# Optimization experiments

Hardware: AMD Instinct MI355X
Metric: run time of the kernel (lower is better)

## Reference

```python
import jax, jax.numpy as jnp
import numpy as np

B, F, N = 64, 32, 36
REGION, HIDDEN, ATT = 1024, 1024, 1024
FEAT2 = REGION + 2 * HIDDEN  # temp_attn feat_size = 3072


def setup_inputs() -> dict:
    key = jax.random.key(0)
    ks = jax.random.split(key, 12)
    s = 0.02
    return {
        "frame_feats": jax.random.normal(ks[0], (B, F, 2 * HIDDEN), jnp.float32),
        "object_feats": jax.random.normal(ks[1], (B, F, N, REGION), jnp.float32),
        "hidden_state": jax.random.normal(ks[2], (B, HIDDEN), jnp.float32),
        # spatial attention params (torch Linear: y = x @ W.T + b)
        "s_wh_w": jax.random.normal(ks[3], (ATT, HIDDEN), jnp.float32) * s,
        "s_wh_b": jnp.zeros((ATT,), jnp.float32),
        "s_wv_w": jax.random.normal(ks[4], (ATT, REGION), jnp.float32) * s,
        "s_wv_b": jnp.zeros((ATT,), jnp.float32),
        "s_wa_w": jax.random.normal(ks[5], (ATT,), jnp.float32) * s,
        # temporal attention params (att_size = hidden_size here)
        "t_wh_w": jax.random.normal(ks[6], (HIDDEN, HIDDEN), jnp.float32) * s,
        "t_wh_b": jnp.zeros((HIDDEN,), jnp.float32),
        "t_wv_w": jax.random.normal(ks[7], (HIDDEN, FEAT2), jnp.float32) * s,
        "t_wv_b": jnp.zeros((HIDDEN,), jnp.float32),
        "t_wa_w": jax.random.normal(ks[8], (HIDDEN,), jnp.float32) * s,
    }


def reference(frame_feats, object_feats, hidden_state,
              s_wh_w, s_wh_b, s_wv_w, s_wv_b, s_wa_w,
              t_wh_w, t_wh_b, t_wv_w, t_wv_b, t_wa_w):
    # ---- spatial attention over num_boxes, per (batch, frame) ----
    # v: [B,F,N,ATT]; key proj broadcasts over frames and boxes
    v = jnp.einsum('bfnd,ad->bfna', object_feats, s_wv_w) + s_wv_b
    h = hidden_state @ s_wh_w.T + s_wh_b            # [B,ATT]
    score = jnp.tanh(v + h[:, None, None, :]) @ s_wa_w  # [B,F,N]
    alpha = jax.nn.softmax(score, axis=-1)
    obj_att = jnp.einsum('bfn,bfnd->bfd', alpha, object_feats)  # [B,F,REGION]

    # ---- temporal attention over frames ----
    feat = jnp.concatenate([obj_att, frame_feats], axis=-1)     # [B,F,FEAT2]
    v2 = jnp.einsum('bfd,ad->bfa', feat, t_wv_w) + t_wv_b       # [B,F,HIDDEN]
    h2 = hidden_state @ t_wh_w.T + t_wh_b                       # [B,HIDDEN]
    score2 = jnp.tanh(v2 + h2[:, None, :]) @ t_wa_w             # [B,F]
    beta = jax.nn.softmax(score2, axis=-1)
    loc_feat = jnp.einsum('bf,bfd->bd', beta, feat)             # [B,FEAT2]
    return loc_feat
```

## Files before the change

kernel.cpp:

```cpp
#include <hip/hip_runtime.h>
#include <hip/hip_bf16.h>
#include <stdint.h>

#define BATCH  64
#define NFRAME 32
#define NBOX   36
#define REGION 1024
#define HIDDEN 1024
#define ATTSZ  1024
#define FEAT2  3072
#define M_S (BATCH * NFRAME * NBOX)
#define M_T (BATCH * NFRAME)

typedef __attribute__((ext_vector_type(8))) short bf16x8;
typedef __attribute__((ext_vector_type(4))) float f32x4;

__device__ __forceinline__ unsigned short f2bf(float f) {
  union { float f; uint32_t u; } v; v.f = f;
  return (unsigned short)((v.u + 0x7FFFu + ((v.u >> 16) & 1u)) >> 16);
}
__device__ __forceinline__ float bf2f(unsigned short u) {
  union { uint32_t u; float f; } v; v.u = (uint32_t)u << 16; return v.f;
}
__device__ __forceinline__ float fast_tanh(float x) {
  float e = __expf(2.f * x);
  return 1.f - 2.f / (e + 1.f);
}
__device__ __forceinline__ void gload_lds16(const unsigned short* g, unsigned short* l) {
  __builtin_amdgcn_global_load_lds(
      (const __attribute__((address_space(1))) unsigned int*)g,
      (__attribute__((address_space(3))) unsigned int*)l, 16, 0, 0);
}

__global__ __launch_bounds__(256) void cast_f32_bf16(
    const float* __restrict__ in, unsigned short* __restrict__ out, long n) {
  long i = ((long)blockIdx.x * 256 + threadIdx.x) * 8;
  if (i >= n) return;
  float4 a = *(const float4*)(in + i);
  float4 b = *(const float4*)(in + i + 4);
  ushort4 lo; lo.x = f2bf(a.x); lo.y = f2bf(a.y); lo.z = f2bf(a.z); lo.w = f2bf(a.w);
  ushort4 hi; hi.x = f2bf(b.x); hi.y = f2bf(b.y); hi.z = f2bf(b.z); hi.w = f2bf(b.w);
  *(ushort4*)(out + i) = lo;
  *(ushort4*)(out + i + 4) = hi;
}

#define BM 128
#define BN 128
#define BK 64

__global__ __launch_bounds__(256) void gemm_tanh_score_bf16(
    const unsigned short* __restrict__ A, const unsigned short* __restrict__ W,
    const float* __restrict__ hvec, const float* __restrict__ wa,
    float* __restrict__ score, int K, int rows_per_b, int n_col_tiles)
{
  __shared__ unsigned short ldsA[BM * BK];
  __shared__ unsigned short ldsW[BN * BK];
  __shared__ float h_tile[4][BN];
  __shared__ float score_sh[2][BM];

  const int tid  = threadIdx.x;
  const int lane = tid & 63;
  const int wid  = tid >> 6;
  const int wr   = (wid >> 1) * 64;
  const int wc   = (wid & 1) * 64;
  const int l15  = lane & 15;
  const int q    = lane >> 4;
  const long r0  = (long)blockIdx.y * BM;
  const int srow = lane >> 3;
  const int sgr  = lane & 7;

  const int b0 = (int)(r0 / rows_per_b);
  const int t1 = (b0 + 1) * rows_per_b - (int)r0;
  const int t2 = t1 + rows_per_b;
  const int t3 = t2 + rows_per_b;

  float sreg[4][4] = {};

  for (int t = 0; t < n_col_tiles; ++t) {
    const int c0 = (blockIdx.x * n_col_tiles + t) * BN;
    __syncthreads();
    for (int idx = tid; idx < 4 * BN; idx += 256) {
      int bl = idx >> 7, c = idx & 127;
      int b = b0 + bl; if (b > BATCH - 1) b = BATCH - 1;
      h_tile[bl][c] = hvec[(long)b * ATTSZ + c0 + c];
    }
    float wac[4];
    #pragma unroll
    for (int j = 0; j < 4; ++j) wac[j] = wa[c0 + wc + j * 16 + l15];

    f32x4 acc[4][4] = {};
    for (int k0 = 0; k0 < K; k0 += BK) {
      __syncthreads();
      #pragma unroll
      for (int it = 0; it < 4; ++it) {
        int c = wid * 4 + it;
        int row = c * 8 + srow;
        gload_lds16(A + (r0 + row) * (long)K + k0 + sgr * 8, ldsA + c * 512);
        gload_lds16(W + (long)(c0 + row) * K + k0 + sgr * 8, ldsW + c * 512);
      }
      __syncthreads();
      #pragma unroll
      for (int s = 0; s < 2; ++s) {
        bf16x8 af[4], wf[4];
        #pragma unroll
        for (int i = 0; i < 4; ++i)
          af[i] = *(const bf16x8*)(ldsA + (wr + i * 16 + l15) * 64 + s * 32 + q * 8);
        #pragma unroll
        for (int j = 0; j < 4; ++j)
          wf[j] = *(const bf16x8*)(ldsW + (wc + j * 16 + l15) * 64 + s * 32 + q * 8);
        #pragma unroll
        for (int i = 0; i < 4; ++i)
          #pragma unroll
          for (int j = 0; j < 4; ++j)
            acc[i][j] = __builtin_amdgcn_mfma_f32_16x16x32_bf16(af[i], wf[j], acc[i][j], 0, 0, 0);
      }
    }
    #pragma unroll
    for (int i = 0; i < 4; ++i) {
      #pragma unroll
      for (int r = 0; r < 4; ++r) {
        int lrow = wr + i * 16 + q * 4 + r;
        int bl = (lrow >= t1) + (lrow >= t2) + (lrow >= t3);
        float part = 0.f;
        #pragma unroll
        for (int j = 0; j < 4; ++j) {
          float x = acc[i][j][r] + h_tile[bl][wc + j * 16 + l15];
          part += fast_tanh(x) * wac[j];
        }
        sreg[i][r] += part;
      }
    }
  }
  #pragma unroll
  for (int i = 0; i < 4; ++i)
    #pragma unroll
    for (int r = 0; r < 4; ++r) {
      float v = sreg[i][r];
      v += __shfl_xor(v, 1); v += __shfl_xor(v, 2);
      v += __shfl_xor(v, 4); v += __shfl_xor(v, 8);
      sreg[i][r] = v;
    }
  if (l15 == 0) {
    #pragma unroll
    for (int i = 0; i < 4; ++i)
      #pragma unroll
      for (int r = 0; r < 4; ++r)
        score_sh[wid & 1][wr + i * 16 + q * 4 + r] = sreg[i][r];
  }
  __syncthreads();
  if (tid < BM)
    atomicAdd(score + r0 + tid, score_sh[0][tid] + score_sh[1][tid]);
}

__global__ __launch_bounds__(256) void hidden_proj(
    const float* __restrict__ hidden,
    const float* __restrict__ s_wh_w, const float* __restrict__ s_wh_b,
    const float* __restrict__ s_wv_b,
    const float* __restrict__ t_wh_w, const float* __restrict__ t_wh_b,
    const float* __restrict__ t_wv_b,
    float* __restrict__ h_s, float* __restrict__ h_t)
{
  const float *W, *b1, *b2;
  float* out;
  if (blockIdx.y == 0) { W = s_wh_w; b1 = s_wh_b; b2 = s_wv_b; out = h_s; }
  else                 { W = t_wh_w; b1 = t_wh_b; b2 = t_wv_b; out = h_t; }
  const int lane = threadIdx.x & 63;
  const int wid  = threadIdx.x >> 6;
  const int a    = blockIdx.x * 4 + wid;
  __shared__ float hs[64 * 256];
  float acc[64];
  #pragma unroll
  for (int b = 0; b < 64; ++b) acc[b] = 0.f;

  for (int dc = 0; dc < 4; ++dc) {
    __syncthreads();
    for (int i = threadIdx.x; i < 4096; i += 256) {
      int b = i >> 6, d4 = i & 63;
      *(float4*)(hs + b * 256 + d4 * 4) =
          *(const float4*)(hidden + b * 1024 + dc * 256 + d4 * 4);
    }
    __syncthreads();
    float4 w4 = *(const float4*)(W + (long)a * 1024 + dc * 256 + lane * 4);
    #pragma unroll
    for (int b = 0; b < 64; ++b) {
      float4 h4 = *(const float4*)(hs + b * 256 + lane * 4);
      acc[b] += w4.x * h4.x + w4.y * h4.y + w4.z * h4.z + w4.w * h4.w;
    }
  }
  #pragma unroll
  for (int b = 0; b < 64; ++b) {
    #pragma unroll
    for (int off = 1; off < 64; off <<= 1)
      acc[b] += __shfl_xor(acc[b], off);
  }
  float res = 0.f;
  #pragma unroll
  for (int b = 0; b < 64; ++b)
    if (lane == b) res = acc[b];
  out[lane * 1024 + a] = res + b1[a] + b2[a];
}

__global__ __launch_bounds__(256) void spatial_softmax_obj_bf16(
    const unsigned short* __restrict__ objb, const float* __restrict__ score,
    const float* __restrict__ frame, float* __restrict__ feat,
    unsigned short* __restrict__ featb)
{
  const int bf = blockIdx.x;
  __shared__ float alpha[NBOX];
  if (threadIdx.x < 64) {
    int n = threadIdx.x;
    float v = (n < NBOX) ? score[bf * NBOX + n] : -1e30f;
    float m = v;
    #pragma unroll
    for (int off = 32; off; off >>= 1) m = fmaxf(m, __shfl_xor(m, off));
    float e = (n < NBOX) ? __expf(v - m) : 0.f;
    float ssum = e;
    #pragma unroll
    for (int off = 32; off; off >>= 1) ssum += __shfl_xor(ssum, off);
    if (n < NBOX) alpha[n] = e / ssum;
  }
  __syncthreads();
  const unsigned short* base = objb + (long)bf * NBOX * REGION;
  float4 av = {0.f, 0.f, 0.f, 0.f};
  for (int n = 0; n < NBOX; ++n) {
    float al = alpha[n];
    ushort4 o = *(const ushort4*)(base + n * REGION + threadIdx.x * 4);
    av.x += al * bf2f(o.x); av.y += al * bf2f(o.y);
    av.z += al * bf2f(o.z); av.w += al * bf2f(o.w);
  }
  float* frow = feat + (long)bf * FEAT2;
  unsigned short* fbrow = featb + (long)bf * FEAT2;
  *(float4*)(frow + threadIdx.x * 4) = av;
  ushort4 avb; avb.x = f2bf(av.x); avb.y = f2bf(av.y); avb.z = f2bf(av.z); avb.w = f2bf(av.w);
  *(ushort4*)(fbrow + threadIdx.x * 4) = avb;
  const float* fsrc = frame + (long)bf * 2 * HIDDEN;
  #pragma unroll
  for (int c = 0; c < 2; ++c) {
    float4 v = *(const float4*)(fsrc + (threadIdx.x + c * 256) * 4);
    *(float4*)(frow + REGION + (threadIdx.x + c * 256) * 4) = v;
    ushort4 vb; vb.x = f2bf(v.x); vb.y = f2bf(v.y); vb.z = f2bf(v.z); vb.w = f2bf(v.w);
    *(ushort4*)(fbrow + REGION + (threadIdx.x + c * 256) * 4) = vb;
  }
}

__global__ __launch_bounds__(256) void temporal_out(
    const float* __restrict__ score2, const float* __restrict__ feat,
    float* __restrict__ out)
{
  const int b = blockIdx.x;
  __shared__ float beta[NFRAME];
  if (threadIdx.x < 64) {
    int f = threadIdx.x;
    float v = (f < NFRAME) ? score2[b * NFRAME + f] : -1e30f;
    float m = v;
    #pragma unroll
    for (int off = 32; off; off >>= 1) m = fmaxf(m, __shfl_xor(m, off));
    float e = (f < NFRAME) ? __expf(v - m) : 0.f;
    float ssum = e;
    #pragma unroll
    for (int off = 32; off; off >>= 1) ssum += __shfl_xor(ssum, off);
    if (f < NFRAME) beta[f] = e / ssum;
  }
  __syncthreads();
  #pragma unroll
  for (int c = 0; c < 3; ++c) {
    int col = (threadIdx.x + c * 256) * 4;
    float4 av = {0.f, 0.f, 0.f, 0.f};
    for (int f = 0; f < NFRAME; ++f) {
      float bw = beta[f];
      float4 v = *(const float4*)(feat + (long)(b * NFRAME + f) * FEAT2 + col);
      av.x += bw * v.x; av.y += bw * v.y; av.z += bw * v.z; av.w += bw * v.w;
    }
    *(float4*)(out + (long)b * FEAT2 + col) = av;
  }
}

#define LDKP 72
__global__ __launch_bounds__(256) void fused_gemm_tanh_score_f32(
    const float* __restrict__ A, const float* __restrict__ W,
    const float* __restrict__ hvec, const float* __restrict__ wa,
    float* __restrict__ score, int M, int K, int rows_per_b)
{
  __shared__ unsigned short ldsA[BM * LDKP];
  __shared__ unsigned short ldsW[BN * LDKP];
  const int tid  = threadIdx.x;
  const int lane = tid & 63;
  const int wid  = tid >> 6;
  const int wr   = (wid >> 1) * 64;
  const int wc   = (wid & 1) * 64;
  const int l15  = lane & 15;
  const int q    = lane >> 4;
  const long r0  = (long)blockIdx.y * BM;
  const int  c0  = blockIdx.x * BN;

  f32x4 acc[4][4] = {};
  for (int k0 = 0; k0 < K; k0 += BK) {
    __syncthreads();
    #pragma unroll
    for (int it = 0; it < 8; ++it) {
      int c = tid + it * 256;
      int row = c >> 4, qb = c & 15;
      float4 s = *(const float4*)(A + (r0 + row) * (long)K + k0 + qb * 4);
      ushort4 d; d.x = f2bf(s.x); d.y = f2bf(s.y); d.z = f2bf(s.z); d.w = f2bf(s.w);
      *(ushort4*)(ldsA + row * LDKP + qb * 4) = d;
    }
    #pragma unroll
    for (int it = 0; it < 8; ++it) {
      int c = tid + it * 256;
      int row = c >> 4, qb = c & 15;
      float4 s = *(const float4*)(W + (c0 + row) * (long)K + k0 + qb * 4);
      ushort4 d; d.x = f2bf(s.x); d.y = f2bf(s.y); d.z = f2bf(s.z); d.w = f2bf(s.w);
      *(ushort4*)(ldsW + row * LDKP + qb * 4) = d;
    }
    __syncthreads();
    #pragma unroll
    for (int s = 0; s < 2; ++s) {
      bf16x8 af[4], bfr[4];
      #pragma unroll
      for (int i = 0; i < 4; ++i)
        af[i] = *(const bf16x8*)(ldsA + (wr + i * 16 + l15) * LDKP + s * 32 + q * 8);
      #pragma unroll
      for (int j = 0; j < 4; ++j)
        bfr[j] = *(const bf16x8*)(ldsW + (wc + j * 16 + l15) * LDKP + s * 32 + q * 8);
      #pragma unroll
      for (int i = 0; i < 4; ++i)
        #pragma unroll
        for (int j = 0; j < 4; ++j)
          acc[i][j] = __builtin_amdgcn_mfma_f32_16x16x32_bf16(af[i], bfr[j], acc[i][j], 0, 0, 0);
    }
  }
  float wac[4];
  #pragma unroll
  for (int j = 0; j < 4; ++j) wac[j] = wa[c0 + wc + j * 16 + l15];
  #pragma unroll
  for (int i = 0; i < 4; ++i) {
    #pragma unroll
    for (int r = 0; r < 4; ++r) {
      int row = (int)r0 + wr + i * 16 + q * 4 + r;
      const float* hrow = hvec + (long)(row / rows_per_b) * ATTSZ;
      float part = 0.f;
      #pragma unroll
      for (int j = 0; j < 4; ++j) {
        float x = acc[i][j][r] + hrow[c0 + wc + j * 16 + l15];
        part += fast_tanh(x) * wac[j];
      }
      part += __shfl_xor(part, 1); part += __shfl_xor(part, 2);
      part += __shfl_xor(part, 4); part += __shfl_xor(part, 8);
      if (l15 == 0) atomicAdd(score + row, part);
    }
  }
}

__global__ __launch_bounds__(256) void spatial_softmax_obj_f32(
    const float* __restrict__ obj, const float* __restrict__ score,
    const float* __restrict__ frame, float* __restrict__ feat)
{
  const int bf = blockIdx.x;
  __shared__ float alpha[NBOX];
  if (threadIdx.x < 64) {
    int n = threadIdx.x;
    float v = (n < NBOX) ? score[bf * NBOX + n] : -1e30f;
    float m = v;
    #pragma unroll
    for (int off = 32; off; off >>= 1) m = fmaxf(m, __shfl_xor(m, off));
    float e = (n < NBOX) ? __expf(v - m) : 0.f;
    float ssum = e;
    #pragma unroll
    for (int off = 32; off; off >>= 1) ssum += __shfl_xor(ssum, off);
    if (n < NBOX) alpha[n] = e / ssum;
  }
  __syncthreads();
  const float* base = obj + (long)bf * NBOX * REGION;
  float4 av = {0.f, 0.f, 0.f, 0.f};
  for (int n = 0; n < NBOX; ++n) {
    float al = alpha[n];
    float4 o = *(const float4*)(base + n * REGION + threadIdx.x * 4);
    av.x += al * o.x; av.y += al * o.y; av.z += al * o.z; av.w += al * o.w;
  }
  float* frow = feat + (long)bf * FEAT2;
  *(float4*)(frow + threadIdx.x * 4) = av;
  const float4* fsrc = (const float4*)(frame + (long)bf * 2 * HIDDEN);
  float4* fdst = (float4*)(frow + REGION);
  fdst[threadIdx.x]       = fsrc[threadIdx.x];
  fdst[threadIdx.x + 256] = fsrc[threadIdx.x + 256];
}

extern "C" void kernel_launch(void* const* d_in, const int* in_sizes, int n_in,
                              void* d_out, int out_size, void* d_ws, size_t ws_size,
                              hipStream_t stream) {
  const float* frame  = (const float*)d_in[0];
  const float* obj    = (const float*)d_in[1];
  const float* hidden = (const float*)d_in[2];
  const float* s_wh_w = (const float*)d_in[3];
  const float* s_wh_b = (const float*)d_in[4];
  const float* s_wv_w = (const float*)d_in[5];
  const float* s_wv_b = (const float*)d_in[6];
  const float* s_wa_w = (const float*)d_in[7];
  const float* t_wh_w = (const float*)d_in[8];
  const float* t_wh_b = (const float*)d_in[9];
  const float* t_wv_w = (const float*)d_in[10];
  const float* t_wv_b = (const float*)d_in[11];
  const float* t_wa_w = (const float*)d_in[12];
  float* out = (float*)d_out;

  char* p = (char*)d_ws;
  auto alloc = [&](size_t bytes) { char* r = p; p += (bytes + 255) & ~255ull; return r; };
  float* h_s     = (float*)alloc(65536 * 4);
  float* h_t     = (float*)alloc(65536 * 4);
  float* score_s = (float*)alloc((size_t)M_S * 4);
  float* score2  = (float*)alloc((size_t)M_T * 4);
  float* feat    = (float*)alloc((size_t)M_T * FEAT2 * 4);
  unsigned short* objb  = (unsigned short*)alloc((size_t)M_S * REGION * 2);
  unsigned short* featb = (unsigned short*)alloc((size_t)M_T * FEAT2 * 2);
  unsigned short* wvsb  = (unsigned short*)alloc((size_t)ATTSZ * REGION * 2);
  unsigned short* wvtb  = (unsigned short*)alloc((size_t)HIDDEN * FEAT2 * 2);
  size_t needed = (size_t)(p - (char*)d_ws);
  bool fast = needed <= ws_size;

  hipMemsetAsync(score_s, 0, (size_t)(M_S + M_T) * sizeof(float), stream);
  hidden_proj<<<dim3(256, 2), 256, 0, stream>>>(
      hidden, s_wh_w, s_wh_b, s_wv_b, t_wh_w, t_wh_b, t_wv_b, h_s, h_t);

  if (fast) {
    cast_f32_bf16<<<(M_S * (long)REGION) / 2048, 256, 0, stream>>>(obj, objb, (long)M_S * REGION);
    cast_f32_bf16<<<(ATTSZ * (long)REGION) / 2048, 256, 0, stream>>>(s_wv_w, wvsb, (long)ATTSZ * REGION);
    cast_f32_bf16<<<(HIDDEN * (long)FEAT2) / 2048, 256, 0, stream>>>(t_wv_w, wvtb, (long)HIDDEN * FEAT2);

    gemm_tanh_score_bf16<<<dim3(2, M_S / BM), 256, 0, stream>>>(
        objb, wvsb, h_s, s_wa_w, score_s, REGION, NFRAME * NBOX, 4);

    spatial_softmax_obj_bf16<<<M_T, 256, 0, stream>>>(objb, score_s, frame, feat, featb);

    gemm_tanh_score_bf16<<<dim3(8, M_T / BM), 256, 0, stream>>>(
        featb, wvtb, h_t, t_wa_w, score2, FEAT2, NFRAME, 1);
  } else {
    fused_gemm_tanh_score_f32<<<dim3(8, M_S / BM), 256, 0, stream>>>(
        obj, s_wv_w, h_s, s_wa_w, score_s, M_S, REGION, NFRAME * NBOX);
    spatial_softmax_obj_f32<<<M_T, 256, 0, stream>>>(obj, score_s, frame, feat);
    fused_gemm_tanh_score_f32<<<dim3(8, M_T / BM), 256, 0, stream>>>(
        feat, t_wv_w, h_t, t_wa_w, score2, M_T, FEAT2, NFRAME);
  }

  temporal_out<<<BATCH, 256, 0, stream>>>(score2, feat, out);
}
```

Before: 911.5 us.

## Template the bf16 GEMM-tanh-score kernel and retile each attention stage

Replaces the fixed 128x128 GEMM-tanh-score kernel with a templated version. Each block now covers one column tile and one batch, so the in-block column-tile loop and the multi-batch hidden-vector handling are gone. The spatial GEMM uses 128x256 tiles, which means each A row-block is re-read fewer times across columns and the grid has more blocks. The temporal GEMM uses 32x128 tiles to launch many more blocks. In exchange, the larger spatial accumulator raises register pressure, and correctness now relies on row tiles never crossing a batch boundary.

```diff
diff --git a/kernel.cpp b/kernel.cpp
--- a/kernel.cpp
+++ b/kernel.cpp
@@ -44,108 +44,84 @@
   *(ushort4*)(out + i + 4) = hi;
 }
 
-#define BM 128
-#define BN 128
-#define BK 64
-
-__global__ __launch_bounds__(256) void gemm_tanh_score_bf16(
+template<int TM, int TN>
+__global__ __launch_bounds__(256, 2) void gemm_tanh_score(
     const unsigned short* __restrict__ A, const unsigned short* __restrict__ W,
     const float* __restrict__ hvec, const float* __restrict__ wa,
-    float* __restrict__ score, int K, int rows_per_b, int n_col_tiles)
-{
-  __shared__ unsigned short ldsA[BM * BK];
-  __shared__ unsigned short ldsW[BN * BK];
-  __shared__ float h_tile[4][BN];
+    float* __restrict__ score, int K, int rows_per_b)
+{
+  constexpr int BM = 2 * TM * 16;
+  constexpr int BN = 2 * TN * 16;
+  __shared__ __align__(16) unsigned short ldsA[BM * 64];
+  __shared__ __align__(16) unsigned short ldsW[BN * 64];
+  __shared__ float h_tile[BN];
   __shared__ float score_sh[2][BM];
 
   const int tid  = threadIdx.x;
   const int lane = tid & 63;
   const int wid  = tid >> 6;
-  const int wr   = (wid >> 1) * 64;
-  const int wc   = (wid & 1) * 64;
+  const int wr   = (wid >> 1) * (TM * 16);
+  const int wc   = (wid & 1) * (TN * 16);
   const int l15  = lane & 15;
   const int q    = lane >> 4;
   const long r0  = (long)blockIdx.y * BM;
+  const int  c0  = blockIdx.x * BN;
   const int srow = lane >> 3;
   const int sgr  = lane & 7;
-
-  const int b0 = (int)(r0 / rows_per_b);
-  const int t1 = (b0 + 1) * rows_per_b - (int)r0;
-  const int t2 = t1 + rows_per_b;
-  const int t3 = t2 + rows_per_b;
-
-  float sreg[4][4] = {};
-
-  for (int t = 0; t < n_col_tiles; ++t) {
-    const int c0 = (blockIdx.x * n_col_tiles + t) * BN;
-    __syncthreads();
-    for (int idx = tid; idx < 4 * BN; idx += 256) {
-      int bl = idx >> 7, c = idx & 127;
-      int b = b0 + bl; if (b > BATCH - 1) b = BATCH - 1;
-      h_tile[bl][c] = hvec[(long)b * ATTSZ + c0 + c];
-    }
-    float wac[4];
-    #pragma unroll
-    for (int j = 0; j < 4; ++j) wac[j] = wa[c0 + wc + j * 16 + l15];
-
-    f32x4 acc[4][4] = {};
-    for (int k0 = 0; k0 < K; k0 += BK) {
-      __syncthreads();
-      #pragma unroll
-      for (int it = 0; it < 4; ++it) {
-        int c = wid * 4 + it;
-        int row = c * 8 + srow;
-        gload_lds16(A + (r0 + row) * (long)K + k0 + sgr * 8, ldsA + c * 512);
-        gload_lds16(W + (long)(c0 + row) * K + k0 + sgr * 8, ldsW + c * 512);
+  const int b0   = (int)(r0 / rows_per_b);
+
+  for (int i = tid; i < BN; i += 256)
+    h_tile[i] = hvec[(long)b0 * ATTSZ + c0 + i];
+  float wac[TN];
+  #pragma unroll
+  for (int j = 0; j < TN; ++j) wac[j] = wa[c0 + wc + j * 16 + l15];
+
+  f32x4 acc[TM][TN] = {};
+
+  for (int k0 = 0; k0 < K; k0 += 64) {
+    __syncthreads();
+    #pragma unroll
+    for (int it = 0; it < BM / 32; ++it) {
+      int c = wid * (BM / 32) + it;
+      gload_lds16(A + (r0 + c * 8 + srow) * (long)K + k0 + sgr * 8, ldsA + c * 512);
+    }
+    #pragma unroll
+    for (int it = 0; it < BN / 32; ++it) {
+      int c = wid * (BN / 32) + it;
+      gload_lds16(W + ((long)(c0 + c * 8 + srow)) * K + k0 + sgr * 8, ldsW + c * 512);
+    }
+    __syncthreads();
+    #pragma unroll
+    for (int s = 0; s < 2; ++s) {
+      bf16x8 af[TM], wf[TN];
+      #pragma unroll
+      for (int i = 0; i < TM; ++i)
+        af[i] = *(const bf16x8*)(ldsA + (wr + i * 16 + l15) * 64 + s * 32 + q * 8);
+      #pragma unroll
+      for (int j = 0; j < TN; ++j)
+        wf[j] = *(const bf16x8*)(ldsW + (wc + j * 16 + l15) * 64 + s * 32 + q * 8);
+      #pragma unroll
+      for (int i = 0; i < TM; ++i)
+        #pragma unroll
+        for (int j = 0; j < TN; ++j)
+          acc[i][j] = __builtin_amdgcn_mfma_f32_16x16x32_bf16(af[i], wf[j], acc[i][j], 0, 0, 0);
+    }
+  }
+
+  #pragma unroll
+  for (int i = 0; i < TM; ++i) {
+    #pragma unroll
+    for (int r = 0; r < 4; ++r) {
+      float part = 0.f;
+      #pragma unroll
+      for (int j = 0; j < TN; ++j) {
+        float x = acc[i][j][r] + h_tile[wc + j * 16 + l15];
+        part += fast_tanh(x) * wac[j];
       }
-      __syncthreads();
-      #pragma unroll
-      for (int s = 0; s < 2; ++s) {
-        bf16x8 af[4], wf[4];
-        #pragma unroll
-        for (int i = 0; i < 4; ++i)
-          af[i] = *(const bf16x8*)(ldsA + (wr + i * 16 + l15) * 64 + s * 32 + q * 8);
-        #pragma unroll
-        for (int j = 0; j < 4; ++j)
-          wf[j] = *(const bf16x8*)(ldsW + (wc + j * 16 + l15) * 64 + s * 32 + q * 8);
-        #pragma unroll
-        for (int i = 0; i < 4; ++i)
-          #pragma unroll
-          for (int j = 0; j < 4; ++j)
-            acc[i][j] = __builtin_amdgcn_mfma_f32_16x16x32_bf16(af[i], wf[j], acc[i][j], 0, 0, 0);
-      }
-    }
-    #pragma unroll
-    for (int i = 0; i < 4; ++i) {
-      #pragma unroll
-      for (int r = 0; r < 4; ++r) {
-        int lrow = wr + i * 16 + q * 4 + r;
-        int bl = (lrow >= t1) + (lrow >= t2) + (lrow >= t3);
-        float part = 0.f;
-        #pragma unroll
-        for (int j = 0; j < 4; ++j) {
-          float x = acc[i][j][r] + h_tile[bl][wc + j * 16 + l15];
-          part += fast_tanh(x) * wac[j];
-        }
-        sreg[i][r] += part;
-      }
-    }
-  }
-  #pragma unroll
-  for (int i = 0; i < 4; ++i)
-    #pragma unroll
-    for (int r = 0; r < 4; ++r) {
-      float v = sreg[i][r];
-      v += __shfl_xor(v, 1); v += __shfl_xor(v, 2);
-      v += __shfl_xor(v, 4); v += __shfl_xor(v, 8);
-      sreg[i][r] = v;
-    }
-  if (l15 == 0) {
-    #pragma unroll
-    for (int i = 0; i < 4; ++i)
-      #pragma unroll
-      for (int r = 0; r < 4; ++r)
-        score_sh[wid & 1][wr + i * 16 + q * 4 + r] = sreg[i][r];
+      part += __shfl_xor(part, 1); part += __shfl_xor(part, 2);
+      part += __shfl_xor(part, 4); part += __shfl_xor(part, 8);
+      if (l15 == 0) score_sh[wid & 1][wr + i * 16 + q * 4 + r] = part;
+    }
   }
   __syncthreads();
   if (tid < BM)
@@ -275,14 +251,17 @@
   }
 }
 
+#define FBM 128
+#define FBN 128
+#define FBK 64
 #define LDKP 72
 __global__ __launch_bounds__(256) void fused_gemm_tanh_score_f32(
     const float* __restrict__ A, const float* __restrict__ W,
     const float* __restrict__ hvec, const float* __restrict__ wa,
     float* __restrict__ score, int M, int K, int rows_per_b)
 {
-  __shared__ unsigned short ldsA[BM * LDKP];
-  __shared__ unsigned short ldsW[BN * LDKP];
+  __shared__ unsigned short ldsA[FBM * LDKP];
+  __shared__ unsigned short ldsW[FBN * LDKP];
   const int tid  = threadIdx.x;
   const int lane = tid & 63;
   const int wid  = tid >> 6;
@@ -290,11 +269,11 @@
   const int wc   = (wid & 1) * 64;
   const int l15  = lane & 15;
   const int q    = lane >> 4;
-  const long r0  = (long)blockIdx.y * BM;
-  const int  c0  = blockIdx.x * BN;
+  const long r0  = (long)blockIdx.y * FBM;
+  const int  c0  = blockIdx.x * FBN;
 
   f32x4 acc[4][4] = {};
-  for (int k0 = 0; k0 < K; k0 += BK) {
+  for (int k0 = 0; k0 < K; k0 += FBK) {
     __syncthreads();
     #pragma unroll
     for (int it = 0; it < 8; ++it) {
@@ -426,18 +405,18 @@
     cast_f32_bf16<<<(ATTSZ * (long)REGION) / 2048, 256, 0, stream>>>(s_wv_w, wvsb, (long)ATTSZ * REGION);
     cast_f32_bf16<<<(HIDDEN * (long)FEAT2) / 2048, 256, 0, stream>>>(t_wv_w, wvtb, (long)HIDDEN * FEAT2);
 
-    gemm_tanh_score_bf16<<<dim3(2, M_S / BM), 256, 0, stream>>>(
-        objb, wvsb, h_s, s_wa_w, score_s, REGION, NFRAME * NBOX, 4);
+    gemm_tanh_score<4, 8><<<dim3(4, M_S / 128), 256, 0, stream>>>(
+        objb, wvsb, h_s, s_wa_w, score_s, REGION, NFRAME * NBOX);
 
     spatial_softmax_obj_bf16<<<M_T, 256, 0, stream>>>(objb, score_s, frame, feat, featb);
 
-    gemm_tanh_score_bf16<<<dim3(8, M_T / BM), 256, 0, stream>>>(
-        featb, wvtb, h_t, t_wa_w, score2, FEAT2, NFRAME, 1);
+    gemm_tanh_score<1, 4><<<dim3(8, M_T / 32), 256, 0, stream>>>(
+        featb, wvtb, h_t, t_wa_w, score2, FEAT2, NFRAME);
   } else {
-    fused_gemm_tanh_score_f32<<<dim3(8, M_S / BM), 256, 0, stream>>>(
+    fused_gemm_tanh_score_f32<<<dim3(8, M_S / FBM), 256, 0, stream>>>(
         obj, s_wv_w, h_s, s_wa_w, score_s, M_S, REGION, NFRAME * NBOX);
     spatial_softmax_obj_f32<<<M_T, 256, 0, stream>>>(obj, score_s, frame, feat);
-    fused_gemm_tanh_score_f32<<<dim3(8, M_T / BM), 256, 0, stream>>>(
+    fused_gemm_tanh_score_f32<<<dim3(8, M_T / FBM), 256, 0, stream>>>(
         feat, t_wv_w, h_t, t_wa_w, score2, M_T, FEAT2, NFRAME);
   }
 
```

Result: faster. 789.5 us (-13.4%).
